# Kernel optimization log

Measured on AMD Instinct MI355X. Metric: run time of the kernel, lower is better.

## Reference

```python
import jax, jax.numpy as jnp
import numpy as np

TEMPERATURE = 0.5
BATCH = 2048  # N = batch_size * world_size (world_size = 1)
FEAT = 128
EPS = 1e-8  # torch CosineSimilarity default eps


def _build_mask_indices(N):
    """Replicates mask_correlated_samples + the row-major boolean gather
    sim[mask].reshape(2N, -1). Returns static flat indices [2N, 2N-1]."""
    sub = np.ones((2 * N, 2 * N), dtype=bool)
    np.fill_diagonal(sub, False)
    idx = np.arange(N)
    sub[idx, N + idx] = False
    sub[N + idx, idx] = False
    mask = np.zeros((3 * N, 3 * N), dtype=bool)
    mask[:2 * N, :2 * N] = sub
    mask[idx, 2 * N + idx] = True
    mask[2 * N + idx, idx] = True
    flat = np.nonzero(mask.ravel())[0]  # row-major order, 2N*(2N-1) entries
    return flat.reshape(2 * N, 2 * N - 1)


_NEG_IDX = jnp.asarray(_build_mask_indices(BATCH), dtype=jnp.int32)


def setup_inputs() -> dict:
    key = jax.random.key(0)
    ka, kp, kn = jax.random.split(key, 3)
    return {
        "anchor": jax.random.normal(ka, (BATCH, FEAT), dtype=jnp.float32),
        "pos": jax.random.normal(kp, (BATCH, FEAT), dtype=jnp.float32),
        "neg": jax.random.normal(kn, (BATCH, FEAT), dtype=jnp.float32),
    }


def reference(anchor, pos, neg):
    N = anchor.shape[0]
    z = jnp.concatenate([anchor, pos, neg], axis=0)  # [3N, d]
    zn = z / jnp.maximum(jnp.linalg.norm(z, axis=1, keepdims=True), EPS)
    sim = (zn @ zn.T) / TEMPERATURE  # [3N, 3N]
    # positive pairs: diagonals at offset +/-2N (anchor<->neg pairs)
    sim_i_j = jnp.diagonal(sim, offset=2 * N)[:N]
    sim_j_i = jnp.diagonal(sim, offset=-2 * N)[:N]
    positive = jnp.concatenate([sim_i_j, sim_j_i]).reshape(2 * N, 1)
    # masked gather of negatives (static index table, row-major order)
    negative = jnp.take(sim.ravel(), _NEG_IDX)  # [2N, 2N-1]
    logits = jnp.concatenate([positive, negative], axis=1)  # [2N, 2N]
    # cross-entropy with label 0, reduction='sum', then / (2N)
    loss = jnp.sum(jax.nn.logsumexp(logits, axis=1) - logits[:, 0]) / (2 * N)
    return loss
```

## Files before the change

### kernel.cpp

```cpp
#include <hip/hip_runtime.h>
#include <hip/hip_bf16.h>

#define N_      2048
#define TWO_N   4096
#define DFEAT   128
#define SCALE   2.0f
#define BROWS   128
#define BCOLS   128
#define NT      (BCOLS / 16)
#define LDSTR   136

typedef __attribute__((ext_vector_type(8))) short bf16x8;
typedef __attribute__((ext_vector_type(4))) float f32x4;

__global__ __launch_bounds__(256) void k_prep(const float* __restrict__ a,
                                              const float* __restrict__ p,
                                              const float* __restrict__ ng,
                                              __hip_bfloat16* __restrict__ zn16,
                                              float* __restrict__ dvec,
                                              float* __restrict__ accS,
                                              float* __restrict__ accP) {
  const int wave = threadIdx.x >> 6;
  const int lane = threadIdx.x & 63;
  const int row  = blockIdx.x * 4 + wave;

  if (threadIdx.x < 4)        accS[blockIdx.x * 4 + threadIdx.x] = 0.0f;
  else if (threadIdx.x < 6)   accP[blockIdx.x * 2 + threadIdx.x - 4] = 0.0f;

  if (row < N_) {
    float2 u = ((const float2*)(a  + (size_t)row * DFEAT))[lane];
    float2 w = ((const float2*)(ng + (size_t)row * DFEAT))[lane];
    float saa = u.x * u.x + u.y * u.y;
    float snn = w.x * w.x + w.y * w.y;
    float san = u.x * w.x + u.y * w.y;
#pragma unroll
    for (int m = 1; m < 64; m <<= 1) {
      saa += __shfl_xor(saa, m);
      snn += __shfl_xor(snn, m);
      san += __shfl_xor(san, m);
    }
    float na = fmaxf(sqrtf(saa), 1e-8f);
    float rn = 1.0f / na;
    __hip_bfloat162 h;
    h.x = __float2bfloat16(u.x * rn);
    h.y = __float2bfloat16(u.y * rn);
    ((__hip_bfloat162*)zn16)[row * (DFEAT / 2) + lane] = h;
    if (lane == 0)
      dvec[row] = SCALE * san / (na * fmaxf(sqrtf(snn), 1e-8f));
  } else {
    float2 v = ((const float2*)(p + (size_t)(row - N_) * DFEAT))[lane];
    float ss = v.x * v.x + v.y * v.y;
#pragma unroll
    for (int m = 1; m < 64; m <<= 1) ss += __shfl_xor(ss, m);
    float rn = 1.0f / fmaxf(sqrtf(ss), 1e-8f);
    __hip_bfloat162 h;
    h.x = __float2bfloat16(v.x * rn);
    h.y = __float2bfloat16(v.y * rn);
    ((__hip_bfloat162*)zn16)[row * (DFEAT / 2) + lane] = h;
  }
}

__global__ __launch_bounds__(256) void k_simsum(const __hip_bfloat16* __restrict__ zn16,
                                                float* __restrict__ accS,
                                                float* __restrict__ accP) {
  const int bx = blockIdx.x, by = blockIdx.y;
  if (by < bx) return;

  __shared__ short Bp[BCOLS * LDSTR];

  const int wave = threadIdx.x >> 6;
  const int lane = threadIdx.x & 63;
  const int lr   = lane & 15;
  const int kg   = lane >> 4;
  const int rb0  = bx * BROWS;
  const int cb0  = by * BCOLS;
  const int rows_base = rb0 + wave * 32;
  const short* zs = (const short*)zn16;

  const bool isDiag    = (bx == by);
  const bool isPartner = (by == bx + 16);
  const bool colP      = (by >= 16) && (bx < by - 16);

  bf16x8 a0[4], a1[4];
#pragma unroll
  for (int kk = 0; kk < 4; ++kk) {
    a0[kk] = *(const bf16x8*)(zs + (size_t)(rows_base + lr) * DFEAT + kk * 32 + kg * 8);
    a1[kk] = *(const bf16x8*)(zs + (size_t)(rows_base + 16 + lr) * DFEAT + kk * 32 + kg * 8);
  }

#pragma unroll
  for (int it = 0; it < 8; ++it) {
    const int g   = it * 256 + threadIdx.x;
    const int col = g >> 4;
    const int q   = g & 15;
    bf16x8 v = *(const bf16x8*)(zs + (size_t)(cb0 + col) * DFEAT + q * 8);
    *(bf16x8*)(&Bp[col * LDSTR + q * 8]) = v;
  }
  __syncthreads();

  float rowS[2][4] = {{0.f,0.f,0.f,0.f},{0.f,0.f,0.f,0.f}};
  const int r0base = rows_base + kg * 4;
  const int r1base = rows_base + 16 + kg * 4;

#pragma unroll 1
  for (int ct = 0; ct < NT; ++ct) {
    bf16x8 b[4];
#pragma unroll
    for (int kk = 0; kk < 4; ++kk)
      b[kk] = *(const bf16x8*)(&Bp[(ct * 16 + lr) * LDSTR + kk * 32 + kg * 8]);

    f32x4 acc0 = {0.f, 0.f, 0.f, 0.f};
    f32x4 acc1 = {0.f, 0.f, 0.f, 0.f};
#pragma unroll
    for (int kk = 0; kk < 4; ++kk) {
      acc0 = __builtin_amdgcn_mfma_f32_16x16x32_bf16(a0[kk], b[kk], acc0, 0, 0, 0);
      acc1 = __builtin_amdgcn_mfma_f32_16x16x32_bf16(a1[kk], b[kk], acc1, 0, 0, 0);
    }

    const int c  = cb0 + ct * 16 + lr;
    const int qc = c - N_;
    float colv = 0.f, colvP = 0.f;

#pragma unroll
    for (int j = 0; j < 4; ++j) {
      const int r0 = r0base + j;
      float e0 = __expf(SCALE * acc0[j]);
      if (isDiag)    e0 = (c  == r0) ? 0.0f : e0;
      if (isPartner) e0 = (qc == r0) ? 0.0f : e0;
      rowS[0][j] += e0;
      if (isPartner) { if (r0 < qc) colvP += e0; else colv += e0; }
      else colv += e0;

      const int r1 = r1base + j;
      float e1 = __expf(SCALE * acc1[j]);
      if (isDiag)    e1 = (c  == r1) ? 0.0f : e1;
      if (isPartner) e1 = (qc == r1) ? 0.0f : e1;
      rowS[1][j] += e1;
      if (isPartner) { if (r1 < qc) colvP += e1; else colv += e1; }
      else colv += e1;
    }

    if (!isDiag) {
      colv += __shfl_xor(colv, 16);
      colv += __shfl_xor(colv, 32);
      if (isPartner) {
        colvP += __shfl_xor(colvP, 16);
        colvP += __shfl_xor(colvP, 32);
        if (kg == 0) {
          atomicAdd(&accS[c], colv);
          atomicAdd(&accP[qc], colvP);
        }
      } else if (kg == 0) {
        if (colP) atomicAdd(&accP[qc], colv);
        else      atomicAdd(&accS[c],  colv);
      }
    }
  }

#pragma unroll
  for (int t = 0; t < 2; ++t)
#pragma unroll
    for (int j = 0; j < 4; ++j) {
      float sv = rowS[t][j];
#pragma unroll
      for (int m = 1; m < 16; m <<= 1) sv += __shfl_xor(sv, m);
      if (lr == 0)
        atomicAdd(&accS[rows_base + t * 16 + kg * 4 + j], sv);
    }
}

__global__ __launch_bounds__(1024) void k_final(const float* __restrict__ dvec,
                                                const float* __restrict__ accS,
                                                const float* __restrict__ accP,
                                                float* __restrict__ out) {
  __shared__ float Elds[N_];
  __shared__ float red[16];
  const int tid = threadIdx.x;
  float dpart = 0.f;
  for (int i = tid; i < N_; i += 1024) {
    float E = __expf(dvec[i]);
    Elds[i] = E;
    dpart += E;
  }
#pragma unroll
  for (int m = 1; m < 64; m <<= 1) dpart += __shfl_xor(dpart, m);
  const int w = tid >> 6, l = tid & 63;
  if (l == 0) red[w] = dpart;
  __syncthreads();
  float Dsum = 0.f;
#pragma unroll
  for (int k = 0; k < 16; ++k) Dsum += red[k];
  __syncthreads();

  float part = 0.f;
  for (int r = tid; r < TWO_N; r += 1024) {
    float S = accS[r];
    float t;
    if (r < N_) {
      t = logf(2.0f * Elds[r] + S) - dvec[r];
    } else {
      const int i = r - N_;
      const float extra = (i < N_ - 1) ? accP[i + 1] : Dsum;
      t = logf(Elds[i] + S + extra) - dvec[i];
    }
    part += t;
  }
#pragma unroll
  for (int m = 1; m < 64; m <<= 1) part += __shfl_xor(part, m);
  if (l == 0) red[w] = part;
  __syncthreads();
  if (tid == 0) {
    float tot = 0.f;
#pragma unroll
    for (int k = 0; k < 16; ++k) tot += red[k];
    out[0] = tot / (float)TWO_N;
  }
}

extern "C" void kernel_launch(void* const* d_in, const int* in_sizes, int n_in,
                              void* d_out, int out_size, void* d_ws, size_t ws_size,
                              hipStream_t stream) {
  const float* a  = (const float*)d_in[0];
  const float* p  = (const float*)d_in[1];
  const float* ng = (const float*)d_in[2];

  char* ws = (char*)d_ws;
  __hip_bfloat16* zn16 = (__hip_bfloat16*)ws;
  float* dvec = (float*)(ws + (size_t)TWO_N * DFEAT * 2);
  float* accS = dvec + TWO_N;
  float* accP = accS + TWO_N;

  k_prep<<<TWO_N / 4, 256, 0, stream>>>(a, p, ng, zn16, dvec, accS, accP);
  k_simsum<<<dim3(TWO_N / BROWS, TWO_N / BCOLS), 256, 0, stream>>>(zn16, accS, accP);
  k_final<<<1, 1024, 0, stream>>>(dvec, accS, accP, (float*)d_out);
}
```

Baseline: 27.75 us.

## Launch only upper-triangular tiles and fuse final reduction via last-block counter

Replaces the 32x32 grid, where half the blocks exit immediately, with a 1D grid of 512 blocks. Each block decodes its upper-triangular tile index, and 16 blocks take one extra tile so all 528 tiles are covered. The separate k_final launch is folded into k_simsum: the last block to finish, detected with an atomic counter, computes the loss. The exp is also switched to exp2 with a prescaled constant and the log to __logf, trading a little accuracy for cheaper instructions.

After: 64.84 us. 2.34x slower.

```diff
diff --git a/kernel.cpp b/kernel.cpp
--- a/kernel.cpp
+++ b/kernel.cpp
@@ -4,14 +4,20 @@
 #define N_      2048
 #define TWO_N   4096
 #define DFEAT   128
-#define SCALE   2.0f
 #define BROWS   128
 #define BCOLS   128
 #define NT      (BCOLS / 16)
 #define LDSTR   136
+#define NBLK    512
+#define NTILES  528
+#define SC_L2E  2.8853900817779268f
 
 typedef __attribute__((ext_vector_type(8))) short bf16x8;
 typedef __attribute__((ext_vector_type(4))) float f32x4;
+
+__device__ __forceinline__ int tri_off(int bx) {
+  return 32 * bx - (bx * (bx - 1)) / 2;
+}
 
 __global__ __launch_bounds__(256) void k_prep(const float* __restrict__ a,
                                               const float* __restrict__ p,
@@ -19,13 +25,15 @@
                                               __hip_bfloat16* __restrict__ zn16,
                                               float* __restrict__ dvec,
                                               float* __restrict__ accS,
-                                              float* __restrict__ accP) {
+                                              float* __restrict__ accP,
+                                              unsigned int* __restrict__ counter) {
   const int wave = threadIdx.x >> 6;
   const int lane = threadIdx.x & 63;
   const int row  = blockIdx.x * 4 + wave;
 
   if (threadIdx.x < 4)        accS[blockIdx.x * 4 + threadIdx.x] = 0.0f;
   else if (threadIdx.x < 6)   accP[blockIdx.x * 2 + threadIdx.x - 4] = 0.0f;
+  if (blockIdx.x == 0 && threadIdx.x == 6) counter[0] = 0u;
 
   if (row < N_) {
     float2 u = ((const float2*)(a  + (size_t)row * DFEAT))[lane];
@@ -46,7 +54,7 @@
     h.y = __float2bfloat16(u.y * rn);
     ((__hip_bfloat162*)zn16)[row * (DFEAT / 2) + lane] = h;
     if (lane == 0)
-      dvec[row] = SCALE * san / (na * fmaxf(sqrtf(snn), 1e-8f));
+      dvec[row] = 2.0f * san / (na * fmaxf(sqrtf(snn), 1e-8f));
   } else {
     float2 v = ((const float2*)(p + (size_t)(row - N_) * DFEAT))[lane];
     float ss = v.x * v.x + v.y * v.y;
@@ -61,160 +69,168 @@
 }
 
 __global__ __launch_bounds__(256) void k_simsum(const __hip_bfloat16* __restrict__ zn16,
+                                                const float* __restrict__ dvec,
                                                 float* __restrict__ accS,
-                                                float* __restrict__ accP) {
-  const int bx = blockIdx.x, by = blockIdx.y;
-  if (by < bx) return;
-
-  __shared__ short Bp[BCOLS * LDSTR];
-
+                                                float* __restrict__ accP,
+                                                unsigned int* __restrict__ counter,
+                                                float* __restrict__ out) {
+  __shared__ __align__(16) short Bp[BCOLS * LDSTR];
+  __shared__ float red[4];
+  __shared__ unsigned int slast;
+
+  const int b    = blockIdx.x;
   const int wave = threadIdx.x >> 6;
   const int lane = threadIdx.x & 63;
   const int lr   = lane & 15;
   const int kg   = lane >> 4;
-  const int rb0  = bx * BROWS;
-  const int cb0  = by * BCOLS;
-  const int rows_base = rb0 + wave * 32;
   const short* zs = (const short*)zn16;
 
-  const bool isDiag    = (bx == by);
-  const bool isPartner = (by == bx + 16);
-  const bool colP      = (by >= 16) && (bx < by - 16);
-
-  bf16x8 a0[4], a1[4];
-#pragma unroll
-  for (int kk = 0; kk < 4; ++kk) {
-    a0[kk] = *(const bf16x8*)(zs + (size_t)(rows_base + lr) * DFEAT + kk * 32 + kg * 8);
-    a1[kk] = *(const bf16x8*)(zs + (size_t)(rows_base + 16 + lr) * DFEAT + kk * 32 + kg * 8);
+  const int textra = ((b & 31) == 16 && (b >> 5) < 16) ? (512 + (b >> 5)) : -1;
+
+  for (int pass = 0; pass < 2; ++pass) {
+    const int t = (pass == 0) ? b : textra;
+    if (t < 0) break;
+
+    int bx = (int)((65.0f - sqrtf(4225.0f - 8.0f * (float)t)) * 0.5f);
+    while (tri_off(bx + 1) <= t) ++bx;
+    while (tri_off(bx) > t) --bx;
+    const int by = bx + (t - tri_off(bx));
+
+    const int rb0 = bx * BROWS;
+    const int cb0 = by * BCOLS;
+    const int rows_base = rb0 + wave * 32;
+
+    const bool isDiag    = (bx == by);
+    const bool isPartner = (by == bx + 16);
+    const bool colP      = (by >= 16) && (bx < by - 16);
+
+    bf16x8 a0[4], a1[4];
+#pragma unroll
+    for (int kk = 0; kk < 4; ++kk) {
+      a0[kk] = *(const bf16x8*)(zs + (size_t)(rows_base + lr) * DFEAT + kk * 32 + kg * 8);
+      a1[kk] = *(const bf16x8*)(zs + (size_t)(rows_base + 16 + lr) * DFEAT + kk * 32 + kg * 8);
+    }
+
+    __syncthreads();
+#pragma unroll
+    for (int it = 0; it < 8; ++it) {
+      const int g   = it * 256 + threadIdx.x;
+      const int col = g >> 4;
+      const int q   = g & 15;
+      bf16x8 v = *(const bf16x8*)(zs + (size_t)(cb0 + col) * DFEAT + q * 8);
+      *(bf16x8*)(&Bp[col * LDSTR + q * 8]) = v;
+    }
+    __syncthreads();
+
+    float rowS[2][4] = {{0.f,0.f,0.f,0.f},{0.f,0.f,0.f,0.f}};
+    const int r0base = rows_base + kg * 4;
+    const int r1base = rows_base + 16 + kg * 4;
+
+#pragma unroll 1
+    for (int ct = 0; ct < NT; ++ct) {
+      bf16x8 bfr[4];
+#pragma unroll
+      for (int kk = 0; kk < 4; ++kk)
+        bfr[kk] = *(const bf16x8*)(&Bp[(ct * 16 + lr) * LDSTR + kk * 32 + kg * 8]);
+
+      f32x4 acc0 = {0.f, 0.f, 0.f, 0.f};
+      f32x4 acc1 = {0.f, 0.f, 0.f, 0.f};
+#pragma unroll
+      for (int kk = 0; kk < 4; ++kk) {
+        acc0 = __builtin_amdgcn_mfma_f32_16x16x32_bf16(a0[kk], bfr[kk], acc0, 0, 0, 0);
+        acc1 = __builtin_amdgcn_mfma_f32_16x16x32_bf16(a1[kk], bfr[kk], acc1, 0, 0, 0);
+      }
+
+      const int c  = cb0 + ct * 16 + lr;
+      const int qc = c - N_;
+      float colv = 0.f, colvP = 0.f;
+
+#pragma unroll
+      for (int j = 0; j < 4; ++j) {
+        const int r0 = r0base + j;
+        float e0 = __builtin_amdgcn_exp2f(acc0[j] * SC_L2E);
+        if (isDiag)    e0 = (c  == r0) ? 0.0f : e0;
+        if (isPartner) e0 = (qc == r0) ? 0.0f : e0;
+        rowS[0][j] += e0;
+        if (isPartner) { if (r0 < qc) colvP += e0; else colv += e0; }
+        else colv += e0;
+
+        const int r1 = r1base + j;
+        float e1 = __builtin_amdgcn_exp2f(acc1[j] * SC_L2E);
+        if (isDiag)    e1 = (c  == r1) ? 0.0f : e1;
+        if (isPartner) e1 = (qc == r1) ? 0.0f : e1;
+        rowS[1][j] += e1;
+        if (isPartner) { if (r1 < qc) colvP += e1; else colv += e1; }
+        else colv += e1;
+      }
+
+      if (!isDiag) {
+        colv += __shfl_xor(colv, 16);
+        colv += __shfl_xor(colv, 32);
+        if (isPartner) {
+          colvP += __shfl_xor(colvP, 16);
+          colvP += __shfl_xor(colvP, 32);
+          if (kg == 0) {
+            atomicAdd(&accS[c], colv);
+            atomicAdd(&accP[qc], colvP);
+          }
+        } else if (kg == 0) {
+          if (colP) atomicAdd(&accP[qc], colv);
+          else      atomicAdd(&accS[c],  colv);
+        }
+      }
+    }
+
+#pragma unroll
+    for (int tt = 0; tt < 2; ++tt)
+#pragma unroll
+      for (int j = 0; j < 4; ++j) {
+        float sv = rowS[tt][j];
+#pragma unroll
+        for (int m = 1; m < 16; m <<= 1) sv += __shfl_xor(sv, m);
+        if (lr == 0)
+          atomicAdd(&accS[rows_base + tt * 16 + kg * 4 + j], sv);
+      }
   }
 
-#pragma unroll
-  for (int it = 0; it < 8; ++it) {
-    const int g   = it * 256 + threadIdx.x;
-    const int col = g >> 4;
-    const int q   = g & 15;
-    bf16x8 v = *(const bf16x8*)(zs + (size_t)(cb0 + col) * DFEAT + q * 8);
-    *(bf16x8*)(&Bp[col * LDSTR + q * 8]) = v;
-  }
-  __syncthreads();
-
-  float rowS[2][4] = {{0.f,0.f,0.f,0.f},{0.f,0.f,0.f,0.f}};
-  const int r0base = rows_base + kg * 4;
-  const int r1base = rows_base + 16 + kg * 4;
-
-#pragma unroll 1
-  for (int ct = 0; ct < NT; ++ct) {
-    bf16x8 b[4];
-#pragma unroll
-    for (int kk = 0; kk < 4; ++kk)
-      b[kk] = *(const bf16x8*)(&Bp[(ct * 16 + lr) * LDSTR + kk * 32 + kg * 8]);
-
-    f32x4 acc0 = {0.f, 0.f, 0.f, 0.f};
-    f32x4 acc1 = {0.f, 0.f, 0.f, 0.f};
-#pragma unroll
-    for (int kk = 0; kk < 4; ++kk) {
-      acc0 = __builtin_amdgcn_mfma_f32_16x16x32_bf16(a0[kk], b[kk], acc0, 0, 0, 0);
-      acc1 = __builtin_amdgcn_mfma_f32_16x16x32_bf16(a1[kk], b[kk], acc1, 0, 0, 0);
-    }
-
-    const int c  = cb0 + ct * 16 + lr;
-    const int qc = c - N_;
-    float colv = 0.f, colvP = 0.f;
-
-#pragma unroll
-    for (int j = 0; j < 4; ++j) {
-      const int r0 = r0base + j;
-      float e0 = __expf(SCALE * acc0[j]);
-      if (isDiag)    e0 = (c  == r0) ? 0.0f : e0;
-      if (isPartner) e0 = (qc == r0) ? 0.0f : e0;
-      rowS[0][j] += e0;
-      if (isPartner) { if (r0 < qc) colvP += e0; else colv += e0; }
-      else colv += e0;
-
-      const int r1 = r1base + j;
-      float e1 = __expf(SCALE * acc1[j]);
-      if (isDiag)    e1 = (c  == r1) ? 0.0f : e1;
-      if (isPartner) e1 = (qc == r1) ? 0.0f : e1;
-      rowS[1][j] += e1;
-      if (isPartner) { if (r1 < qc) colvP += e1; else colv += e1; }
-      else colv += e1;
-    }
-
-    if (!isDiag) {
-      colv += __shfl_xor(colv, 16);
-      colv += __shfl_xor(colv, 32);
-      if (isPartner) {
-        colvP += __shfl_xor(colvP, 16);
-        colvP += __shfl_xor(colvP, 32);
-        if (kg == 0) {
-          atomicAdd(&accS[c], colv);
-          atomicAdd(&accP[qc], colvP);
-        }
-      } else if (kg == 0) {
-        if (colP) atomicAdd(&accP[qc], colv);
-        else      atomicAdd(&accS[c],  colv);
-      }
-    }
-  }
-
-#pragma unroll
-  for (int t = 0; t < 2; ++t)
-#pragma unroll
-    for (int j = 0; j < 4; ++j) {
-      float sv = rowS[t][j];
-#pragma unroll
-      for (int m = 1; m < 16; m <<= 1) sv += __shfl_xor(sv, m);
-      if (lr == 0)
-        atomicAdd(&accS[rows_base + t * 16 + kg * 4 + j], sv);
-    }
-}
-
-__global__ __launch_bounds__(1024) void k_final(const float* __restrict__ dvec,
-                                                const float* __restrict__ accS,
-                                                const float* __restrict__ accP,
-                                                float* __restrict__ out) {
-  __shared__ float Elds[N_];
-  __shared__ float red[16];
+  __threadfence();
+  __syncthreads();
+  if (threadIdx.x == 0)
+    slast = __hip_atomic_fetch_add(counter, 1u, __ATOMIC_ACQ_REL,
+                                   __HIP_MEMORY_SCOPE_AGENT);
+  __syncthreads();
+  if (slast != NBLK - 1) return;
+  __threadfence();
+
   const int tid = threadIdx.x;
   float dpart = 0.f;
-  for (int i = tid; i < N_; i += 1024) {
-    float E = __expf(dvec[i]);
-    Elds[i] = E;
-    dpart += E;
-  }
+  for (int i = tid; i < N_; i += 256) dpart += __expf(dvec[i]);
 #pragma unroll
   for (int m = 1; m < 64; m <<= 1) dpart += __shfl_xor(dpart, m);
-  const int w = tid >> 6, l = tid & 63;
-  if (l == 0) red[w] = dpart;
-  __syncthreads();
-  float Dsum = 0.f;
-#pragma unroll
-  for (int k = 0; k < 16; ++k) Dsum += red[k];
+  if (lane == 0) red[wave] = dpart;
+  __syncthreads();
+  const float Dsum = red[0] + red[1] + red[2] + red[3];
   __syncthreads();
 
   float part = 0.f;
-  for (int r = tid; r < TWO_N; r += 1024) {
+  for (int r = tid; r < TWO_N; r += 256) {
     float S = accS[r];
-    float t;
+    float v;
     if (r < N_) {
-      t = logf(2.0f * Elds[r] + S) - dvec[r];
+      v = __logf(2.0f * __expf(dvec[r]) + S) - dvec[r];
     } else {
       const int i = r - N_;
       const float extra = (i < N_ - 1) ? accP[i + 1] : Dsum;
-      t = logf(Elds[i] + S + extra) - dvec[i];
-    }
-    part += t;
+      v = __logf(__expf(dvec[i]) + S + extra) - dvec[i];
+    }
+    part += v;
   }
 #pragma unroll
   for (int m = 1; m < 64; m <<= 1) part += __shfl_xor(part, m);
-  if (l == 0) red[w] = part;
-  __syncthreads();
-  if (tid == 0) {
-    float tot = 0.f;
-#pragma unroll
-    for (int k = 0; k < 16; ++k) tot += red[k];
-    out[0] = tot / (float)TWO_N;
-  }
+  if (lane == 0) red[wave] = part;
+  __syncthreads();
+  if (tid == 0)
+    out[0] = (red[0] + red[1] + red[2] + red[3]) / (float)TWO_N;
 }
 
 extern "C" void kernel_launch(void* const* d_in, const int* in_sizes, int n_in,
@@ -229,8 +245,8 @@
   float* dvec = (float*)(ws + (size_t)TWO_N * DFEAT * 2);
   float* accS = dvec + TWO_N;
   float* accP = accS + TWO_N;
-
-  k_prep<<<TWO_N / 4, 256, 0, stream>>>(a, p, ng, zn16, dvec, accS, accP);
-  k_simsum<<<dim3(TWO_N / BROWS, TWO_N / BCOLS), 256, 0, stream>>>(zn16, accS, accP);
-  k_final<<<1, 1024, 0, stream>>>(dvec, accS, accP, (float*)d_out);
-}
+  unsigned int* counter = (unsigned int*)(accP + N_);
+
+  k_prep<<<TWO_N / 4, 256, 0, stream>>>(a, p, ng, zn16, dvec, accS, accP, counter);
+  k_simsum<<<NBLK, 256, 0, stream>>>(zn16, dvec, accS, accP, counter, (float*)d_out);
+}
```
